# Performance work log

Hardware: AMD Instinct MI355X
Metric: run time of the kernel (lower is better)

## Reference

```python
import jax, jax.numpy as jnp
import numpy as np

IMG = 128                  # img_size
FMM = 35.0
SENSOR = 32.0
FUV = FMM * IMG / SENSOR   # focal length in pixels (screen space, in_ndc=False)
N_PTS = 16384
CHUNK = 1024               # points per scan step
R_SIL = 0.008              # silhouette pass radius (NDC)
R_DEP = 0.012              # depth pass radius (NDC)
K_SIL = 8
K_DEP = 16
DIST = 1.2


def _look_at(dist, elev_deg, azim_deg):
    # PyTorch3D look_at_view_transform with at=origin, up=+Y, degrees=True
    elev = jnp.deg2rad(elev_deg)
    azim = jnp.deg2rad(azim_deg)
    cam = jnp.stack([dist * jnp.cos(elev) * jnp.sin(azim),
                     dist * jnp.sin(elev),
                     dist * jnp.cos(elev) * jnp.cos(azim)], axis=-1)  # (B,3)
    up = jnp.array([0.0, 1.0, 0.0], dtype=cam.dtype)
    z_ax = -cam / (jnp.linalg.norm(cam, axis=-1, keepdims=True) + 1e-8)
    x_ax = jnp.cross(jnp.broadcast_to(up, z_ax.shape), z_ax)
    x_ax = x_ax / (jnp.linalg.norm(x_ax, axis=-1, keepdims=True) + 1e-8)
    y_ax = jnp.cross(z_ax, x_ax)
    R = jnp.stack([x_ax, y_ax, z_ax], axis=-1)   # columns are camera axes
    T = -jnp.einsum('bi,bij->bj', cam, R)        # X_cam = X_world @ R + T
    return R, T


def _project(pts, R, T):
    # world -> camera (row-vector convention) -> screen px -> PyTorch3D NDC
    Xc = jnp.einsum('bni,bij->bnj', pts, R) + T[:, None, :]
    z = Xc[..., 2]
    z_safe = jnp.where(z > 1e-5, z, 1.0)  # points behind camera are culled anyway
    xs = FUV * Xc[..., 0] / z_safe + IMG / 2.0
    ys = FUV * Xc[..., 1] / z_safe + IMG / 2.0
    x_ndc = 1.0 - 2.0 * xs / IMG
    y_ndc = 1.0 - 2.0 * ys / IMG
    return jnp.stack([x_ndc, y_ndc], axis=-1), z


def _rasterize(xy, z, r2, K):
    """Per-pixel K nearest-in-depth points within per-point NDC radius.
    xy: (B,N,2) NDC, z: (B,N) camera depth, r2: (B,N) squared radius.
    Returns zbuf, dists of shape (B,IMG,IMG,K), -1 for empty slots."""
    B, N, _ = xy.shape
    P = IMG * IMG
    # pixel-center NDC grid (PyTorch3D: +X left, +Y up; row-major flatten)
    gxs = 1.0 - (2.0 * jnp.arange(IMG, dtype=xy.dtype) + 1.0) / IMG  # per column
    gys = 1.0 - (2.0 * jnp.arange(IMG, dtype=xy.dtype) + 1.0) / IMG  # per row
    gx = jnp.tile(gxs, IMG)          # (P,)
    gy = jnp.repeat(gys, IMG)        # (P,)

    nch = N // CHUNK
    px = xy[..., 0].reshape(B, nch, CHUNK).swapaxes(0, 1)
    py = xy[..., 1].reshape(B, nch, CHUNK).swapaxes(0, 1)
    pz = z.reshape(B, nch, CHUNK).swapaxes(0, 1)
    pr2 = r2.reshape(B, nch, CHUNK).swapaxes(0, 1)

    def body(carry, c):
        top_z, top_d = carry
        cx, cy, cz, cr2 = c                               # each (B,CHUNK)
        dx = gx[None, :, None] - cx[:, None, :]           # (B,P,CHUNK)
        dy = gy[None, :, None] - cy[:, None, :]
        d2 = dx * dx + dy * dy
        ok = (d2 < cr2[:, None, :]) & (cz[:, None, :] > 0.0)
        zc = jnp.where(ok, cz[:, None, :], jnp.inf)
        cand_z = jnp.concatenate([top_z, zc], axis=-1)    # (B,P,K+CHUNK)
        cand_d = jnp.concatenate([top_d, d2], axis=-1)
        negz, idx = jax.lax.top_k(-cand_z, K)             # K smallest depths
        return (-negz, jnp.take_along_axis(cand_d, idx, axis=-1)), None

    init = (jnp.full((B, P, K), jnp.inf, dtype=xy.dtype),
            jnp.zeros((B, P, K), dtype=xy.dtype))
    (top_z, top_d), _ = jax.lax.scan(jax.checkpoint(body), init, (px, py, pz, pr2))
    valid = jnp.isfinite(top_z)
    zbuf = jnp.where(valid, top_z, -1.0).reshape(B, IMG, IMG, K)
    dists = jnp.where(valid, top_d, -1.0).reshape(B, IMG, IMG, K)
    return zbuf, dists


def setup_inputs() -> dict:
    key = jax.random.key(0)
    k1, k2 = jax.random.split(key)
    point_cloud = jax.random.normal(k1, (2, N_PTS, 6), dtype=jnp.float32) * 0.25
    param = jax.random.normal(k2, (2, 8, 3), dtype=jnp.float32) * 20.0  # degrees
    return {"point_cloud": point_cloud, "param": param}


def reference(point_cloud, param):
    pts = point_cloud[..., :3]
    B = pts.shape[0]
    elev0 = param[:, 1, 0]
    azim0 = param[:, 0, 0]

    # ---- silhouette pass (radius 0.008, K=8) + alpha compositing ----
    R0, T0 = _look_at(DIST, elev0, azim0)
    xy0, z0 = _project(pts, R0, T0)
    r2_sil = jnp.full((B, N_PTS), R_SIL * R_SIL, dtype=pts.dtype)
    _, dists_s = _rasterize(xy0, z0, r2_sil, K_SIL)
    alphas = jnp.where(dists_s >= 0.0, 1.0 - dists_s / (R_SIL * R_SIL), 0.0)
    trans = jnp.cumprod(1.0 - alphas, axis=-1)
    trans_excl = jnp.concatenate([jnp.ones_like(trans[..., :1]), trans[..., :-1]], axis=-1)
    sihlt_map = jnp.sum(alphas * trans_excl, axis=-1, keepdims=True) * 255.0  # (B,H,W,1)

    # ---- depth pass with random view (radius 0.012, K=16) ----
    kd = jax.random.key(42)
    ke, ka = jax.random.split(kd)
    elev_d = jax.random.uniform(ke, (B,), dtype=pts.dtype) * 60.0 - 30.0
    azim_d = jax.random.uniform(ka, (B,), dtype=pts.dtype) * 300.0 + azim0 + 30.0
    Rd, Td = _look_at(DIST, elev_d, azim_d)
    xyd, zd = _project(pts, Rd, Td)
    r2_dep = jnp.full((B, N_PTS), R_DEP * R_DEP, dtype=pts.dtype)
    zbuf_d, _ = _rasterize(xyd, zd, r2_dep, K_DEP)
    depth_ini = zbuf_d[..., 0]

    # density-aware adaptive radius (detached, per source .detach())
    area = jnp.sum((jax.lax.stop_gradient(depth_ini) > 0.0).astype(pts.dtype), axis=(1, 2))
    pa_radius = area / 16384.0 * 0.057                      # (B,)
    r2_ada = jnp.broadcast_to((pa_radius * pa_radius)[:, None], (B, N_PTS))

    zbuf_a, dists_a = _rasterize(xyd, zd, r2_ada, K_DEP)
    depth_img = zbuf_a[..., :8]
    dist_top = dists_a[..., :8]
    return (sihlt_map, depth_img, dist_top)
```

## Files before the change

kernel.cpp:

```cpp
#include <hip/hip_runtime.h>
#include <cstring>
#include <cstdint>

#define NPTS 16384
#define FUVC 140.0f
#define R_SILF 0.008f
#define R_DEPF 0.012f
#define R2_SIL (0.008f*0.008f)
#define R2_DEP (0.012f*0.012f)
#define CH 512

#define AREA_OFF  48
#define PA_OFF    50
#define R2ADA_OFF 52
#define CNT_SIL   64
#define OFF_SIL   2112
#define CNT_ADA   4160
#define OFF_ADA   6208
#define FLAGS8    8256
#define FLAGS     8256
#define ZERO_END  16448
#define PROJ0     41024
#define PROJ1     172096
#define LSILF     303168
#define LADAF     827456
#define WS1_WORDS 2007104u
#define WS1_NEEDED ((size_t)WS1_WORDS * 4u)
#define LSIL      303168
#define LADA      434240
#define WS2_WORDS 729152u
#define WS2_NEEDED ((size_t)WS2_WORDS * 4u)

__device__ __forceinline__ void cam_calc(float elev, float azim, float c[12]) {
    const float D2R = 0.017453292519943295f;
    float er = elev * D2R, ar = azim * D2R;
    float ce = cosf(er), se = sinf(er), ca = cosf(ar), sa = sinf(ar);
    float cx = 1.2f * ce * sa, cy = 1.2f * se, cz = 1.2f * ce * ca;
    float n = sqrtf(cx*cx + cy*cy + cz*cz) + 1e-8f;
    float zx = -cx / n, zy = -cy / n, zz = -cz / n;
    float xx = zz, xy = 0.0f, xz = -zx;
    float xn = sqrtf(xx*xx + xy*xy + xz*xz) + 1e-8f;
    xx /= xn; xz /= xn;
    float yx = zy*xz - zz*xy, yy = zz*xx - zx*xz, yz = zx*xy - zy*xx;
    c[0]=xx; c[1]=xy; c[2]=xz; c[3]=yx; c[4]=yy; c[5]=yz;
    c[6]=zx; c[7]=zy; c[8]=zz;
    c[9]  = -(cx*xx + cy*xy + cz*xz);
    c[10] = -(cx*yx + cy*yy + cz*yz);
    c[11] = -(cx*zx + cy*zy + cz*zz);
}

__device__ __forceinline__ void cam_compute(const float* __restrict__ param,
                                            float* __restrict__ ws,
                                            int t, float ue0, float ue1,
                                            float ua0, float ua1) {
    int b = t >> 1, cam = t & 1;
    float azim0 = param[b * 24 + 0];
    float elev0 = param[b * 24 + 3];
    float elev, azim;
    if (cam == 0) { elev = elev0; azim = azim0; }
    else {
        float ue = b ? ue1 : ue0;
        float ua = b ? ua1 : ua0;
        elev = ue * 60.0f - 30.0f;
        azim = ua * 300.0f + azim0 + 30.0f;
    }
    float c[12];
    cam_calc(elev, azim, c);
    float* w = ws + t * 12;
    #pragma unroll
    for (int i = 0; i < 12; i++) w[i] = c[i];
}

__device__ __forceinline__ float4 project_pt(const float* __restrict__ P,
                                             const float c[12]) {
    float X = P[0], Y = P[1], Z = P[2];
    float xc = X*c[0] + Y*c[1] + Z*c[2] + c[9];
    float yc = X*c[3] + Y*c[4] + Z*c[5] + c[10];
    float zc = X*c[6] + Y*c[7] + Z*c[8] + c[11];
    float zs = zc > 1e-5f ? zc : 1.0f;
    float px = 1.0f - (FUVC * xc / zs + 64.0f) * (1.0f/64.0f);
    float py = 1.0f - (FUVC * yc / zs + 64.0f) * (1.0f/64.0f);
    return make_float4(px, py, zc, 0.0f);
}

__device__ __forceinline__ void pix_range(float p, float r, int& lo, int& hi) {
    float lo_f = (1.0f - p - r) * 64.0f - 0.5f;
    float hi_f = (1.0f - p + r) * 64.0f - 0.5f;
    lo = (int)ceilf(lo_f - 1e-3f);
    hi = (int)floorf(hi_f + 1e-3f);
    lo = max(lo, 0); hi = min(hi, 127);
}

__device__ __forceinline__ void top8_insert(float z, float d,
                                            float tz[8], float td[8]) {
    #pragma unroll
    for (int k = 0; k < 8; k++) {
        bool lt = z < tz[k];
        float oz = tz[k], od = td[k];
        if (lt) { tz[k] = z; td[k] = d; z = oz; d = od; }
    }
}

__device__ __forceinline__ void hit_test(float4 pt, float gx, float gy, float r2,
                                         float tz[8], float td[8]) {
    float dx = gx - pt.x, dy = gy - pt.y;
    float d2 = dx*dx + dy*dy;
    if (d2 < r2 && pt.z > 0.0f && pt.z < tz[7]) top8_insert(pt.z, d2, tz, td);
}

__device__ __forceinline__ void merge_sorted8(float tz[8], float td[8], int mask) {
    float oz[8], od[8];
    #pragma unroll
    for (int k = 0; k < 8; k++) {
        oz[k] = __shfl_xor(tz[k], mask);
        od[k] = __shfl_xor(td[k], mask);
    }
    float mz[8], md[8];
    #pragma unroll
    for (int k = 0; k < 8; k++) {
        bool take = oz[7 - k] < tz[k];
        mz[k] = take ? oz[7 - k] : tz[k];
        md[k] = take ? od[7 - k] : td[k];
    }
    #define CE(i, j) { bool sw = mz[j] < mz[i]; \
        float t1 = mz[i], t2 = md[i]; \
        mz[i] = sw ? mz[j] : mz[i]; md[i] = sw ? md[j] : md[i]; \
        mz[j] = sw ? t1 : mz[j];    md[j] = sw ? t2 : md[j]; }
    CE(0,4) CE(1,5) CE(2,6) CE(3,7)
    CE(0,2) CE(1,3) CE(4,6) CE(5,7)
    CE(0,1) CE(2,3) CE(4,5) CE(6,7)
    #undef CE
    #pragma unroll
    for (int k = 0; k < 8; k++) { tz[k] = mz[k]; td[k] = md[k]; }
}

__device__ __forceinline__ void scan1024(unsigned* uw, unsigned cbase,
                                         unsigned obase, unsigned* s, int t) {
    unsigned c0 = uw[cbase + t*4 + 0];
    unsigned c1 = uw[cbase + t*4 + 1];
    unsigned c2 = uw[cbase + t*4 + 2];
    unsigned c3 = uw[cbase + t*4 + 3];
    unsigned tot = c0 + c1 + c2 + c3;
    s[t] = tot; __syncthreads();
    for (int off = 1; off < 256; off <<= 1) {
        unsigned v = (t >= off) ? s[t - off] : 0u;
        __syncthreads();
        s[t] += v;
        __syncthreads();
    }
    unsigned base = s[t] - tot;
    uw[obase + t*4 + 0] = base;
    uw[obase + t*4 + 1] = base + c0;
    uw[obase + t*4 + 2] = base + c0 + c1;
    uw[obase + t*4 + 3] = base + c0 + c1 + c2;
    uw[cbase + t*4 + 0] = 0;
    uw[cbase + t*4 + 1] = 0;
    uw[cbase + t*4 + 2] = 0;
    uw[cbase + t*4 + 3] = 0;
}


__global__ __launch_bounds__(256) void k_zero(float* __restrict__ ws) {
    unsigned* uw = (unsigned*)ws;
    int gid = blockIdx.x * 256 + threadIdx.x;
    int stride = gridDim.x * 256;
    for (int i = gid; i < ZERO_END; i += stride) uw[i] = 0u;
}

__global__ __launch_bounds__(256) void k_proj_v3(const float* __restrict__ pc,
                                                 const float* __restrict__ param,
                                                 float* __restrict__ ws,
                                                 float ue0, float ue1,
                                                 float ua0, float ua1) {
    unsigned* uw = (unsigned*)ws;
    unsigned char* fb = (unsigned char*)(uw + FLAGS8);
    int b = blockIdx.x >> 6;
    int p = ((blockIdx.x & 63) << 8) + threadIdx.x;
    const float* P = pc + ((size_t)b * NPTS + p) * 6;

    float azim0 = param[b * 24 + 0];
    float elev0 = param[b * 24 + 3];
    float c0[12], c1[12];
    cam_calc(elev0, azim0, c0);
    float ue = b ? ue1 : ue0;
    float ua = b ? ua1 : ua0;
    cam_calc(ue * 60.0f - 30.0f, ua * 300.0f + azim0 + 30.0f, c1);

    float4 q0 = project_pt(P, c0);
    ((float4*)(ws + PROJ0))[b * NPTS + p] = q0;
    if (q0.z > 0.0f) {
        int cl, chh, rl, rh;
        pix_range(q0.x, R_SILF, cl, chh);
        pix_range(q0.y, R_SILF, rl, rh);
        if (cl <= chh && rl <= rh) {
            int bxl = cl >> 2, bxh = chh >> 2, byl = rl >> 2, byh = rh >> 2;
            for (int by = byl; by <= byh; by++)
                for (int bx = bxl; bx <= bxh; bx++)
                    atomicAdd(&uw[CNT_SIL + b * 1024 + by * 32 + bx], 1u);
        }
    }

    float4 q1 = project_pt(P, c1);
    ((float4*)(ws + PROJ1))[b * NPTS + p] = q1;
    if (q1.z > 0.0f) {
        int cl, chh, rl, rh;
        pix_range(q1.x, R_DEPF, cl, chh);
        pix_range(q1.y, R_DEPF, rl, rh);
        for (int rr = rl; rr <= rh; rr++) {
            float gy = 1.0f - (float)(2 * rr + 1) * (1.0f/128.0f);
            float dy = gy - q1.y;
            for (int cc = cl; cc <= chh; cc++) {
                float gx = 1.0f - (float)(2 * cc + 1) * (1.0f/128.0f);
                float dx = gx - q1.x;
                float d2 = dx*dx + dy*dy;
                if (d2 < R2_DEP) fb[b * NPTS + rr * 128 + cc] = 1;
            }
        }
    }
}

__global__ __launch_bounds__(256) void k_area_scan_v3(float* __restrict__ ws) {
    unsigned* uw = (unsigned*)ws;
    __shared__ unsigned s[256];
    int t = threadIdx.x;
    int job = blockIdx.x;
    if (job < 2) {
        int b = job;
        unsigned acc = 0;
        #pragma unroll
        for (int j = 0; j < 16; j++) {
            unsigned w = uw[FLAGS8 + b * 4096 + t * 16 + j];
            acc += __popc(w & 0x01010101u);
        }
        s[t] = acc; __syncthreads();
        for (int off = 128; off > 0; off >>= 1) {
            if (t < off) s[t] += s[t + off];
            __syncthreads();
        }
        if (t == 0) {
            unsigned area = s[0];
            uw[AREA_OFF + b] = area;
            float pa = (float)area * (1.0f/16384.0f) * 0.057f;
            ws[PA_OFF + b] = pa;
            ws[R2ADA_OFF + b] = pa * pa;
        }
    } else {
        int b = job - 2;
        scan1024(uw, CNT_SIL + b * 1024, OFF_SIL + b * 1024, s, t);
    }
}

__global__ __launch_bounds__(64) void k_cntada_scatsil(float* __restrict__ ws) {
    unsigned* uw = (unsigned*)ws;
    int id = blockIdx.x;
    bool isCnt = id < 512;
    int p = ((isCnt ? id : id - 512) << 6) + threadIdx.x;
    int b = p >> 14;
    if (isCnt) {
        float4 q = ((const float4*)(ws + PROJ1))[p];
        float pa = ws[PA_OFF + b];
        if (q.z > 0.0f) {
            int cl, chh, rl, rh;
            pix_range(q.x, pa, cl, chh);
            pix_range(q.y, pa, rl, rh);
            if (cl <= chh && rl <= rh) {
                int bxl = cl >> 2, bxh = chh >> 2, byl = rl >> 2, byh = rh >> 2;
                for (int by = byl; by <= byh; by++)
                    for (int bx = bxl; bx <= bxh; bx++)
                        atomicAdd(&uw[CNT_ADA + b * 1024 + by * 32 + bx], 1u);
            }
        }
    } else {
        float4 q = ((const float4*)(ws + PROJ0))[p];
        if (q.z > 0.0f) {
            int cl, chh, rl, rh;
            pix_range(q.x, R_SILF, cl, chh);
            pix_range(q.y, R_SILF, rl, rh);
            if (cl <= chh && rl <= rh) {
                int bxl = cl >> 2, bxh = chh >> 2, byl = rl >> 2, byh = rh >> 2;
                for (int by = byl; by <= byh; by++)
                    for (int bx = bxl; bx <= bxh; bx++) {
                        unsigned bin = b * 1024 + by * 32 + bx;
                        unsigned idx = uw[OFF_SIL + bin] + atomicAdd(&uw[CNT_SIL + bin], 1u);
                        ((float4*)(ws + LSILF))[b * 65536 + idx] = q;
                    }
            }
        }
    }
}

__global__ __launch_bounds__(64) void k_scan_ada64(float* __restrict__ ws) {
    unsigned* uw = (unsigned*)ws;
    int b = blockIdx.x;
    int t = threadIdx.x;
    unsigned c[16]; unsigned tot = 0;
    #pragma unroll
    for (int j = 0; j < 16; j++) { c[j] = uw[CNT_ADA + b * 1024 + t * 16 + j]; tot += c[j]; }
    unsigned inc = tot;
    #pragma unroll
    for (int off = 1; off < 64; off <<= 1) {
        unsigned v = __shfl_up(inc, off);
        if (t >= off) inc += v;
    }
    unsigned base = inc - tot;
    #pragma unroll
    for (int j = 0; j < 16; j++) {
        uw[OFF_ADA + b * 1024 + t * 16 + j] = base;
        base += c[j];
        uw[CNT_ADA + b * 1024 + t * 16 + j] = 0u;
    }
}

__global__ __launch_bounds__(64) void k_scatter_ada_v2(float* __restrict__ ws) {
    unsigned* uw = (unsigned*)ws;
    int p = (blockIdx.x << 6) + threadIdx.x;
    int b = p >> 14;
    float4 q = ((const float4*)(ws + PROJ1))[p];
    float pa = ws[PA_OFF + b];
    if (q.z > 0.0f) {
        int cl, chh, rl, rh;
        pix_range(q.x, pa, cl, chh);
        pix_range(q.y, pa, rl, rh);
        if (cl <= chh && rl <= rh) {
            int bxl = cl >> 2, bxh = chh >> 2, byl = rl >> 2, byh = rh >> 2;
            for (int by = byl; by <= byh; by++)
                for (int bx = bxl; bx <= bxh; bx++) {
                    unsigned bin = b * 1024 + by * 32 + bx;
                    unsigned idx = uw[OFF_ADA + bin] + atomicAdd(&uw[CNT_ADA + bin], 1u);
                    ((float4*)(ws + LADAF))[b * 147456 + idx] = q;
                }
        }
    }
}

__global__ __launch_bounds__(64) void k_gather_v3(const float* __restrict__ ws,
                                                  float* __restrict__ out) {
    const unsigned* uw = (const unsigned*)ws;
    int id = blockIdx.x;
    bool sil = id < 2048;
    int gt = sil ? id : id - 2048;
    int b = gt >> 10;
    int tile = gt & 1023;
    int lane = threadIdx.x;
    int p = lane & 15, s = lane >> 4;
    int bx = tile & 31, by = tile >> 5;
    int col = (bx << 2) + (p & 3), row = (by << 2) + (p >> 2);
    float gx = 1.0f - (float)(2*col + 1) * (1.0f/128.0f);
    float gy = 1.0f - (float)(2*row + 1) * (1.0f/128.0f);
    float r2 = sil ? R2_SIL : ws[R2ADA_OFF + b];
    unsigned start = sil ? uw[OFF_SIL + b * 1024 + tile] : uw[OFF_ADA + b * 1024 + tile];
    unsigned len   = sil ? uw[CNT_SIL + b * 1024 + tile] : uw[CNT_ADA + b * 1024 + tile];
    const float4* lst = sil ? ((const float4*)(ws + LSILF)) + b * 65536 + start
                            : ((const float4*)(ws + LADAF)) + b * 147456 + start;

    float tz[8], td[8];
    #pragma unroll
    for (int k = 0; k < 8; k++) { tz[k] = INFINITY; td[k] = 0.0f; }

    unsigned i = (unsigned)s;
    while (i + 28 < len) {
        float4 cb[8];
        #pragma unroll
        for (int u = 0; u < 8; u++) cb[u] = lst[i + 4u * (unsigned)u];
        #pragma unroll
        for (int u = 0; u < 8; u++) hit_test(cb[u], gx, gy, r2, tz, td);
        i += 32;
    }
    for (; i < len; i += 4) hit_test(lst[i], gx, gy, r2, tz, td);

    merge_sorted8(tz, td, 16);
    merge_sorted8(tz, td, 32);

    if (s == 0) {
        int pix = (b << 14) + row * 128 + col;
        if (sil) {
            float trans = 1.0f, acc = 0.0f;
            #pragma unroll
            for (int k = 0; k < 8; k++) {
                float a = (tz[k] != INFINITY) ? (1.0f - td[k] / R2_SIL) : 0.0f;
                acc += a * trans;
                trans *= (1.0f - a);
            }
            out[pix] = acc * 255.0f;
        } else {
            float* dep = out + 32768  + (size_t)pix * 8;
            float* dst = out + 294912 + (size_t)pix * 8;
            #pragma unroll
            for (int k = 0; k < 8; k++) {
                bool v = (tz[k] != INFINITY);
                dep[k] = v ? tz[k] : -1.0f;
                dst[k] = v ? td[k] : -1.0f;
            }
        }
    }
}


__global__ __launch_bounds__(256) void k_init(const float* __restrict__ param,
                                              float* __restrict__ ws,
                                              float ue0, float ue1,
                                              float ua0, float ua1) {
    unsigned* uw = (unsigned*)ws;
    int gid = blockIdx.x * 256 + threadIdx.x;
    int stride = gridDim.x * 256;
    for (int i = gid; i < 2048; i += stride) { uw[CNT_SIL + i] = 0u; uw[CNT_ADA + i] = 0u; }
    for (int i = gid; i < 32768; i += stride) uw[FLAGS + i] = 0u;
    if (gid < 2) uw[AREA_OFF + gid] = 0u;
    if (gid < 4) cam_compute(param, ws, gid, ue0, ue1, ua0, ua1);
}

__global__ __launch_bounds__(256) void k_proj_count(const float* __restrict__ pc,
                                                    float* __restrict__ ws) {
    unsigned* uw = (unsigned*)ws;
    int b = blockIdx.x >> 6;
    int p = ((blockIdx.x & 63) << 8) + threadIdx.x;
    const float* P = pc + ((size_t)b * NPTS + p) * 6;
    float c0[12], c1[12];
    const float* w0 = ws + (b * 2) * 12;
    #pragma unroll
    for (int i = 0; i < 12; i++) { c0[i] = w0[i]; c1[i] = w0[12 + i]; }

    float4 q0 = project_pt(P, c0);
    ((float4*)(ws + PROJ0))[b * NPTS + p] = q0;
    if (q0.z > 0.0f) {
        int cl, chh, rl, rh;
        pix_range(q0.x, R_SILF, cl, chh);
        pix_range(q0.y, R_SILF, rl, rh);
        if (cl <= chh && rl <= rh) {
            int bxl = cl >> 2, bxh = chh >> 2, byl = rl >> 2, byh = rh >> 2;
            for (int by = byl; by <= byh; by++)
                for (int bx = bxl; bx <= bxh; bx++)
                    atomicAdd(&uw[CNT_SIL + b * 1024 + by * 32 + bx], 1u);
        }
    }

    float4 q1 = project_pt(P, c1);
    ((float4*)(ws + PROJ1))[b * NPTS + p] = q1;
    if (q1.z > 0.0f) {
        int cl, chh, rl, rh;
        pix_range(q1.x, R_DEPF, cl, chh);
        pix_range(q1.y, R_DEPF, rl, rh);
        for (int rr = rl; rr <= rh; rr++) {
            float gy = 1.0f - (float)(2 * rr + 1) * (1.0f/128.0f);
            float dy = gy - q1.y;
            for (int cc = cl; cc <= chh; cc++) {
                float gx = 1.0f - (float)(2 * cc + 1) * (1.0f/128.0f);
                float dx = gx - q1.x;
                float d2 = dx*dx + dy*dy;
                if (d2 < R2_DEP) uw[FLAGS + b * NPTS + rr * 128 + cc] = 1u;
            }
        }
    }
}

__global__ __launch_bounds__(256) void k_area_scan(float* __restrict__ ws) {
    unsigned* uw = (unsigned*)ws;
    __shared__ unsigned s[256];
    int t = threadIdx.x;
    int job = blockIdx.x;
    if (job < 2) {
        int b = job;
        unsigned acc = 0;
        for (int i = t; i < NPTS; i += 256) acc += uw[FLAGS + b * NPTS + i];
        s[t] = acc; __syncthreads();
        for (int off = 128; off > 0; off >>= 1) {
            if (t < off) s[t] += s[t + off];
            __syncthreads();
        }
        if (t == 0) {
            unsigned area = s[0];
            uw[AREA_OFF + b] = area;
            float pa = (float)area * (1.0f/16384.0f) * 0.057f;
            ws[PA_OFF + b] = pa;
            ws[R2ADA_OFF + b] = pa * pa;
        }
    } else {
        int b = job - 2;
        scan1024(uw, CNT_SIL + b * 1024, OFF_SIL + b * 1024, s, t);
    }
}

__global__ __launch_bounds__(256) void k_count_ada(float* __restrict__ ws) {
    unsigned* uw = (unsigned*)ws;
    int b = blockIdx.x >> 6;
    int p = ((blockIdx.x & 63) << 8) + threadIdx.x;
    float4 q = ((const float4*)(ws + PROJ1))[b * NPTS + p];
    float pa = ws[PA_OFF + b];
    if (q.z > 0.0f) {
        int cl, chh, rl, rh;
        pix_range(q.x, pa, cl, chh);
        pix_range(q.y, pa, rl, rh);
        if (cl <= chh && rl <= rh) {
            int bxl = cl >> 2, bxh = chh >> 2, byl = rl >> 2, byh = rh >> 2;
            for (int by = byl; by <= byh; by++)
                for (int bx = bxl; bx <= bxh; bx++)
                    atomicAdd(&uw[CNT_ADA + b * 1024 + by * 32 + bx], 1u);
        }
    }
}

__global__ __launch_bounds__(256) void k_scan_ada(float* __restrict__ ws) {
    unsigned* uw = (unsigned*)ws;
    __shared__ unsigned s[256];
    int b = blockIdx.x;
    scan1024(uw, CNT_ADA + b * 1024, OFF_ADA + b * 1024, s, threadIdx.x);
}

__global__ __launch_bounds__(256) void k_scatter(float* __restrict__ ws) {
    unsigned* uw = (unsigned*)ws;
    int b = blockIdx.x >> 6;
    int p = ((blockIdx.x & 63) << 8) + threadIdx.x;

    float4 q0 = ((const float4*)(ws + PROJ0))[b * NPTS + p];
    if (q0.z > 0.0f) {
        int cl, chh, rl, rh;
        pix_range(q0.x, R_SILF, cl, chh);
        pix_range(q0.y, R_SILF, rl, rh);
        if (cl <= chh && rl <= rh) {
            int bxl = cl >> 2, bxh = chh >> 2, byl = rl >> 2, byh = rh >> 2;
            for (int by = byl; by <= byh; by++)
                for (int bx = bxl; bx <= bxh; bx++) {
                    unsigned bin = b * 1024 + by * 32 + bx;
                    unsigned idx = uw[OFF_SIL + bin] + atomicAdd(&uw[CNT_SIL + bin], 1u);
                    uw[LSIL + b * 65536 + idx] = (unsigned)p;
                }
        }
    }

    float4 q1 = ((const float4*)(ws + PROJ1))[b * NPTS + p];
    float pa = ws[PA_OFF + b];
    if (q1.z > 0.0f) {
        int cl, chh, rl, rh;
        pix_range(q1.x, pa, cl, chh);
        pix_range(q1.y, pa, rl, rh);
        if (cl <= chh && rl <= rh) {
            int bxl = cl >> 2, bxh = chh >> 2, byl = rl >> 2, byh = rh >> 2;
            for (int by = byl; by <= byh; by++)
                for (int bx = bxl; bx <= bxh; bx++) {
                    unsigned bin = b * 1024 + by * 32 + bx;
                    unsigned idx = uw[OFF_ADA + bin] + atomicAdd(&uw[CNT_ADA + bin], 1u);
                    uw[LADA + b * 147456 + idx] = (unsigned)p;
                }
        }
    }
}

__global__ __launch_bounds__(256) void k_gather_sil(const float* __restrict__ ws,
                                                    float* __restrict__ out) {
    const unsigned* uw = (const unsigned*)ws;
    int b = blockIdx.x >> 6;
    int tile = (blockIdx.x & 63) * 16 + (threadIdx.x >> 4);
    int q = threadIdx.x & 15;
    int bx = tile & 31, by = tile >> 5;
    int col = (bx << 2) + (q & 3), row = (by << 2) + (q >> 2);
    float gx = 1.0f - (float)(2*col + 1) * (1.0f/128.0f);
    float gy = 1.0f - (float)(2*row + 1) * (1.0f/128.0f);
    unsigned start = uw[OFF_SIL + b * 1024 + tile];
    unsigned len   = uw[CNT_SIL + b * 1024 + tile];
    const float4* pr = (const float4*)(ws + PROJ0) + b * NPTS;

    float tz[8], td[8];
    #pragma unroll
    for (int k = 0; k < 8; k++) { tz[k] = INFINITY; td[k] = 0.0f; }
    for (unsigned i = 0; i < len; i++) {
        unsigned pid = uw[LSIL + b * 65536 + start + i];
        hit_test(pr[pid], gx, gy, R2_SIL, tz, td);
    }
    float trans = 1.0f, s = 0.0f;
    #pragma unroll
    for (int k = 0; k < 8; k++) {
        float a = (tz[k] != INFINITY) ? (1.0f - td[k] / R2_SIL) : 0.0f;
        s += a * trans;
        trans *= (1.0f - a);
    }
    out[(b << 14) + row * 128 + col] = s * 255.0f;
}

__global__ __launch_bounds__(256) void k_gather_ada(const float* __restrict__ ws,
                                                    float* __restrict__ out) {
    const unsigned* uw = (const unsigned*)ws;
    int b = blockIdx.x >> 6;
    int tile = (blockIdx.x & 63) * 16 + (threadIdx.x >> 4);
    int q = threadIdx.x & 15;
    int bx = tile & 31, by = tile >> 5;
    int col = (bx << 2) + (q & 3), row = (by << 2) + (q >> 2);
    float gx = 1.0f - (float)(2*col + 1) * (1.0f/128.0f);
    float gy = 1.0f - (float)(2*row + 1) * (1.0f/128.0f);
    float r2 = ws[R2ADA_OFF + b];
    unsigned start = uw[OFF_ADA + b * 1024 + tile];
    unsigned len   = uw[CNT_ADA + b * 1024 + tile];
    const float4* pr = (const float4*)(ws + PROJ1) + b * NPTS;

    float tz[8], td[8];
    #pragma unroll
    for (int k = 0; k < 8; k++) { tz[k] = INFINITY; td[k] = 0.0f; }
    for (unsigned i = 0; i < len; i++) {
        unsigned pid = uw[LADA + b * 147456 + start + i];
        hit_test(pr[pid], gx, gy, r2, tz, td);
    }
    int pix = (b << 14) + row * 128 + col;
    float* dep = out + 32768  + (size_t)pix * 8;
    float* dst = out + 294912 + (size_t)pix * 8;
    #pragma unroll
    for (int k = 0; k < 8; k++) {
        bool v = (tz[k] != INFINITY);
        dep[k] = v ? tz[k] : -1.0f;
        dst[k] = v ? td[k] : -1.0f;
    }
}

__global__ void cam_kernel_fb(const float* __restrict__ param, float* __restrict__ ws,
                              float ue0, float ue1, float ua0, float ua1) {
    int t = threadIdx.x;
    if (t < 2) ws[48 + t] = 0.0f;
    if (t >= 4) return;
    cam_compute(param, ws, t, ue0, ue1, ua0, ua1);
}

__device__ __forceinline__ void stage_points(const float* __restrict__ pcb,
                                             const float c[12], int c0, float4* sp) {
    for (int i = threadIdx.x; i < CH; i += 256) {
        const float* P = pcb + (size_t)(c0 + i) * 6;
        sp[i] = project_pt(P, c);
    }
}

__global__ __launch_bounds__(256) void raster_AB(const float* __restrict__ pc,
                                                 float* __restrict__ ws,
                                                 float* __restrict__ out) {
    __shared__ float4 sp[CH];
    int bid = blockIdx.x;
    bool silMode = bid < 128;
    int q = silMode ? bid : bid - 128;
    int b = q >> 6;
    int p = ((q & 63) << 8) + threadIdx.x;
    const float* cw = ws + (b * 2 + (silMode ? 0 : 1)) * 12;
    float c[12];
    #pragma unroll
    for (int i = 0; i < 12; i++) c[i] = cw[i];
    float r2 = silMode ? R2_SIL : R2_DEP;
    int col = p & 127, row = p >> 7;
    float gx = 1.0f - (float)(2*col + 1) * (1.0f/128.0f);
    float gy = 1.0f - (float)(2*row + 1) * (1.0f/128.0f);
    const float* pcb = pc + (size_t)b * NPTS * 6;

    if (silMode) {
        float tz[8], td[8];
        #pragma unroll
        for (int k = 0; k < 8; k++) { tz[k] = INFINITY; td[k] = 0.0f; }
        for (int c0 = 0; c0 < NPTS; c0 += CH) {
            __syncthreads();
            stage_points(pcb, c, c0, sp);
            __syncthreads();
            #pragma unroll 4
            for (int j = 0; j < CH; j++) hit_test(sp[j], gx, gy, r2, tz, td);
        }
        float trans = 1.0f, s = 0.0f;
        #pragma unroll
        for (int k = 0; k < 8; k++) {
            float a = (tz[k] != INFINITY) ? (1.0f - td[k] / r2) : 0.0f;
            s += a * trans;
            trans *= (1.0f - a);
        }
        out[(b << 14) + p] = s * 255.0f;
    } else {
        float mz = INFINITY;
        for (int c0 = 0; c0 < NPTS; c0 += CH) {
            __syncthreads();
            stage_points(pcb, c, c0, sp);
            __syncthreads();
            #pragma unroll 4
            for (int j = 0; j < CH; j++) {
                float4 pt = sp[j];
                float dx = gx - pt.x, dy = gy - pt.y;
                float d2 = dx*dx + dy*dy;
                if (d2 < r2 && pt.z > 0.0f) mz = fminf(mz, pt.z);
            }
        }
        unsigned long long m = __ballot(mz != INFINITY);
        if ((threadIdx.x & 63) == 0)
            atomicAdd(ws + 48 + b, (float)__popcll(m));
    }
}

__global__ __launch_bounds__(256) void raster_C(const float* __restrict__ pc,
                                                const float* __restrict__ ws,
                                                float* __restrict__ out) {
    __shared__ float4 sp[CH];
    int bid = blockIdx.x;
    int b = bid >> 6;
    int p = ((bid & 63) << 8) + threadIdx.x;
    const float* cw = ws + (b * 2 + 1) * 12;
    float c[12];
    #pragma unroll
    for (int i = 0; i < 12; i++) c[i] = cw[i];
    float area = ws[48 + b];
    float pa = (area * (1.0f/16384.0f)) * 0.057f;
    float r2 = pa * pa;
    int col = p & 127, row = p >> 7;
    float gx = 1.0f - (float)(2*col + 1) * (1.0f/128.0f);
    float gy = 1.0f - (float)(2*row + 1) * (1.0f/128.0f);
    const float* pcb = pc + (size_t)b * NPTS * 6;

    float tz[8], td[8];
    #pragma unroll
    for (int k = 0; k < 8; k++) { tz[k] = INFINITY; td[k] = 0.0f; }
    for (int c0 = 0; c0 < NPTS; c0 += CH) {
        __syncthreads();
        stage_points(pcb, c, c0, sp);
        __syncthreads();
        #pragma unroll 4
        for (int j = 0; j < CH; j++) hit_test(sp[j], gx, gy, r2, tz, td);
    }
    float* dep = out + 32768  + (size_t)((b << 14) + p) * 8;
    float* dst = out + 294912 + (size_t)((b << 14) + p) * 8;
    #pragma unroll
    for (int k = 0; k < 8; k++) {
        bool v = (tz[k] != INFINITY);
        dep[k] = v ? tz[k] : -1.0f;
        dst[k] = v ? td[k] : -1.0f;
    }
}

static inline uint32_t rotl32(uint32_t x, int r) { return (x << r) | (x >> (32 - r)); }

static void tf2x32(uint32_t k0, uint32_t k1, uint32_t c0, uint32_t c1,
                   uint32_t* o0, uint32_t* o1) {
    uint32_t ks0 = k0, ks1 = k1, ks2 = k0 ^ k1 ^ 0x1BD11BDAu;
    uint32_t x0 = c0 + ks0, x1 = c1 + ks1;
    static const int rA[4] = {13, 15, 26, 6};
    static const int rB[4] = {17, 29, 16, 24};
    #define RND4(R) do { for (int i = 0; i < 4; i++) { x0 += x1; x1 = rotl32(x1, R[i]); x1 ^= x0; } } while (0)
    RND4(rA); x0 += ks1; x1 += ks2 + 1u;
    RND4(rB); x0 += ks2; x1 += ks0 + 2u;
    RND4(rA); x0 += ks0; x1 += ks1 + 3u;
    RND4(rB); x0 += ks1; x1 += ks2 + 4u;
    RND4(rA); x0 += ks2; x1 += ks0 + 5u;
    #undef RND4
    *o0 = x0; *o1 = x1;
}

static inline float bits_to_unit_float(uint32_t bits) {
    uint32_t fb = (bits >> 9) | 0x3f800000u;
    float f;
    memcpy(&f, &fb, 4);
    return f - 1.0f;
}

extern "C" void kernel_launch(void* const* d_in, const int* in_sizes, int n_in,
                              void* d_out, int out_size, void* d_ws, size_t ws_size,
                              hipStream_t stream) {
    const float* pc    = (const float*)d_in[0];
    const float* param = (const float*)d_in[1];
    float* out = (float*)d_out;
    float* ws  = (float*)d_ws;

    uint32_t ke0, ke1, ka0, ka1, b1, b2;
    tf2x32(0u, 42u, 0u, 0u, &ke0, &ke1);
    tf2x32(0u, 42u, 0u, 1u, &ka0, &ka1);
    float ue[2], ua[2];
    for (uint32_t i = 0; i < 2; i++) {
        tf2x32(ke0, ke1, 0u, i, &b1, &b2);
        ue[i] = bits_to_unit_float(b1 ^ b2);
        tf2x32(ka0, ka1, 0u, i, &b1, &b2);
        ua[i] = bits_to_unit_float(b1 ^ b2);
    }

    if (ws_size >= WS1_NEEDED) {
        k_zero          <<<16, 256, 0, stream>>>(ws);
        k_proj_v3       <<<128, 256, 0, stream>>>(pc, param, ws, ue[0], ue[1], ua[0], ua[1]);
        k_area_scan_v3  <<<4, 256, 0, stream>>>(ws);
        k_cntada_scatsil<<<1024, 64, 0, stream>>>(ws);
        k_scan_ada64    <<<2, 64, 0, stream>>>(ws);
        k_scatter_ada_v2<<<512, 64, 0, stream>>>(ws);
        k_gather_v3     <<<4096, 64, 0, stream>>>(ws, out);
    } else if (ws_size >= WS2_NEEDED) {
        k_init      <<<64, 256, 0, stream>>>(param, ws, ue[0], ue[1], ua[0], ua[1]);
        k_proj_count<<<128, 256, 0, stream>>>(pc, ws);
        k_area_scan <<<4, 256, 0, stream>>>(ws);
        k_count_ada <<<128, 256, 0, stream>>>(ws);
        k_scan_ada  <<<2, 256, 0, stream>>>(ws);
        k_scatter   <<<128, 256, 0, stream>>>(ws);
        k_gather_sil<<<128, 256, 0, stream>>>(ws, out);
        k_gather_ada<<<128, 256, 0, stream>>>(ws, out);
    } else {
        cam_kernel_fb<<<1, 64, 0, stream>>>(param, ws, ue[0], ue[1], ua[0], ua[1]);
        raster_AB<<<256, 256, 0, stream>>>(pc, ws, out);
        raster_C <<<128, 256, 0, stream>>>(pc, ws, out);
    }
}
```

Before: 96.44 us.

## Fuse seven-kernel pipeline into one cooperative kernel with grid syncs

Replaces the chain of seven kernel launches (zero, project, area/scan, count/scatter, scan, scatter, gather) with a single cooperative kernel of 1024 blocks that separates the stages with grid.sync(). The goal is to remove per-launch overhead and inter-kernel gaps, which dominate a workload this small. In exchange it adds grid-wide barrier cost, runs many idle threads in the serial scan stages, and queries device properties and occupancy on the host every call. It falls back to the old launches if cooperative launch is unavailable.

```diff
diff --git a/kernel.cpp b/kernel.cpp
--- a/kernel.cpp
+++ b/kernel.cpp
@@ -1,6 +1,9 @@
 #include <hip/hip_runtime.h>
+#include <hip/hip_cooperative_groups.h>
 #include <cstring>
 #include <cstdint>
+
+namespace cg = cooperative_groups;
 
 #define NPTS 16384
 #define FUVC 140.0f
@@ -31,6 +34,9 @@
 #define WS2_WORDS 729152u
 #define WS2_NEEDED ((size_t)WS2_WORDS * 4u)
 
+#define FUSED_BLOCKS 1024
+#define FUSED_NT (FUSED_BLOCKS * 256)
+
 __device__ __forceinline__ void cam_calc(float elev, float azim, float c[12]) {
     const float D2R = 0.017453292519943295f;
     float er = elev * D2R, ar = azim * D2R;
@@ -159,32 +165,15 @@
     uw[cbase + t*4 + 3] = 0;
 }
 
-
-__global__ __launch_bounds__(256) void k_zero(float* __restrict__ ws) {
-    unsigned* uw = (unsigned*)ws;
-    int gid = blockIdx.x * 256 + threadIdx.x;
-    int stride = gridDim.x * 256;
-    for (int i = gid; i < ZERO_END; i += stride) uw[i] = 0u;
-}
-
-__global__ __launch_bounds__(256) void k_proj_v3(const float* __restrict__ pc,
-                                                 const float* __restrict__ param,
-                                                 float* __restrict__ ws,
-                                                 float ue0, float ue1,
-                                                 float ua0, float ua1) {
+__device__ __forceinline__ void body_proj(const float* __restrict__ pc,
+                                          float* __restrict__ ws, int b, int p) {
     unsigned* uw = (unsigned*)ws;
     unsigned char* fb = (unsigned char*)(uw + FLAGS8);
-    int b = blockIdx.x >> 6;
-    int p = ((blockIdx.x & 63) << 8) + threadIdx.x;
     const float* P = pc + ((size_t)b * NPTS + p) * 6;
-
-    float azim0 = param[b * 24 + 0];
-    float elev0 = param[b * 24 + 3];
     float c0[12], c1[12];
-    cam_calc(elev0, azim0, c0);
-    float ue = b ? ue1 : ue0;
-    float ua = b ? ua1 : ua0;
-    cam_calc(ue * 60.0f - 30.0f, ua * 300.0f + azim0 + 30.0f, c1);
+    const float* w0 = ws + (b * 2) * 12;
+    #pragma unroll
+    for (int i = 0; i < 12; i++) { c0[i] = w0[i]; c1[i] = w0[12 + i]; }
 
     float4 q0 = project_pt(P, c0);
     ((float4*)(ws + PROJ0))[b * NPTS + p] = q0;
@@ -219,11 +208,9 @@
     }
 }
 
-__global__ __launch_bounds__(256) void k_area_scan_v3(float* __restrict__ ws) {
-    unsigned* uw = (unsigned*)ws;
-    __shared__ unsigned s[256];
-    int t = threadIdx.x;
-    int job = blockIdx.x;
+__device__ __forceinline__ void body_area_scan(float* __restrict__ ws, int job,
+                                               int t, unsigned* s) {
+    unsigned* uw = (unsigned*)ws;
     if (job < 2) {
         int b = job;
         unsigned acc = 0;
@@ -250,49 +237,46 @@
     }
 }
 
-__global__ __launch_bounds__(64) void k_cntada_scatsil(float* __restrict__ ws) {
-    unsigned* uw = (unsigned*)ws;
-    int id = blockIdx.x;
-    bool isCnt = id < 512;
-    int p = ((isCnt ? id : id - 512) << 6) + threadIdx.x;
+__device__ __forceinline__ void body_cnt_ada(float* __restrict__ ws, int p) {
+    unsigned* uw = (unsigned*)ws;
     int b = p >> 14;
-    if (isCnt) {
-        float4 q = ((const float4*)(ws + PROJ1))[p];
-        float pa = ws[PA_OFF + b];
-        if (q.z > 0.0f) {
-            int cl, chh, rl, rh;
-            pix_range(q.x, pa, cl, chh);
-            pix_range(q.y, pa, rl, rh);
-            if (cl <= chh && rl <= rh) {
-                int bxl = cl >> 2, bxh = chh >> 2, byl = rl >> 2, byh = rh >> 2;
-                for (int by = byl; by <= byh; by++)
-                    for (int bx = bxl; bx <= bxh; bx++)
-                        atomicAdd(&uw[CNT_ADA + b * 1024 + by * 32 + bx], 1u);
-            }
-        }
-    } else {
-        float4 q = ((const float4*)(ws + PROJ0))[p];
-        if (q.z > 0.0f) {
-            int cl, chh, rl, rh;
-            pix_range(q.x, R_SILF, cl, chh);
-            pix_range(q.y, R_SILF, rl, rh);
-            if (cl <= chh && rl <= rh) {
-                int bxl = cl >> 2, bxh = chh >> 2, byl = rl >> 2, byh = rh >> 2;
-                for (int by = byl; by <= byh; by++)
-                    for (int bx = bxl; bx <= bxh; bx++) {
-                        unsigned bin = b * 1024 + by * 32 + bx;
-                        unsigned idx = uw[OFF_SIL + bin] + atomicAdd(&uw[CNT_SIL + bin], 1u);
-                        ((float4*)(ws + LSILF))[b * 65536 + idx] = q;
-                    }
-            }
-        }
-    }
-}
-
-__global__ __launch_bounds__(64) void k_scan_ada64(float* __restrict__ ws) {
-    unsigned* uw = (unsigned*)ws;
-    int b = blockIdx.x;
-    int t = threadIdx.x;
+    float4 q = ((const float4*)(ws + PROJ1))[p];
+    float pa = ws[PA_OFF + b];
+    if (q.z > 0.0f) {
+        int cl, chh, rl, rh;
+        pix_range(q.x, pa, cl, chh);
+        pix_range(q.y, pa, rl, rh);
+        if (cl <= chh && rl <= rh) {
+            int bxl = cl >> 2, bxh = chh >> 2, byl = rl >> 2, byh = rh >> 2;
+            for (int by = byl; by <= byh; by++)
+                for (int bx = bxl; bx <= bxh; bx++)
+                    atomicAdd(&uw[CNT_ADA + b * 1024 + by * 32 + bx], 1u);
+        }
+    }
+}
+
+__device__ __forceinline__ void body_scat_sil(float* __restrict__ ws, int p) {
+    unsigned* uw = (unsigned*)ws;
+    int b = p >> 14;
+    float4 q = ((const float4*)(ws + PROJ0))[p];
+    if (q.z > 0.0f) {
+        int cl, chh, rl, rh;
+        pix_range(q.x, R_SILF, cl, chh);
+        pix_range(q.y, R_SILF, rl, rh);
+        if (cl <= chh && rl <= rh) {
+            int bxl = cl >> 2, bxh = chh >> 2, byl = rl >> 2, byh = rh >> 2;
+            for (int by = byl; by <= byh; by++)
+                for (int bx = bxl; bx <= bxh; bx++) {
+                    unsigned bin = b * 1024 + by * 32 + bx;
+                    unsigned idx = uw[OFF_SIL + bin] + atomicAdd(&uw[CNT_SIL + bin], 1u);
+                    ((float4*)(ws + LSILF))[b * 65536 + idx] = q;
+                }
+        }
+    }
+}
+
+__device__ __forceinline__ void body_scan_ada(float* __restrict__ ws, int b, int t) {
+    unsigned* uw = (unsigned*)ws;
     unsigned c[16]; unsigned tot = 0;
     #pragma unroll
     for (int j = 0; j < 16; j++) { c[j] = uw[CNT_ADA + b * 1024 + t * 16 + j]; tot += c[j]; }
@@ -311,9 +295,8 @@
     }
 }
 
-__global__ __launch_bounds__(64) void k_scatter_ada_v2(float* __restrict__ ws) {
-    unsigned* uw = (unsigned*)ws;
-    int p = (blockIdx.x << 6) + threadIdx.x;
+__device__ __forceinline__ void body_scat_ada(float* __restrict__ ws, int p) {
+    unsigned* uw = (unsigned*)ws;
     int b = p >> 14;
     float4 q = ((const float4*)(ws + PROJ1))[p];
     float pa = ws[PA_OFF + b];
@@ -333,15 +316,14 @@
     }
 }
 
-__global__ __launch_bounds__(64) void k_gather_v3(const float* __restrict__ ws,
-                                                  float* __restrict__ out) {
+__device__ __forceinline__ void body_gather(const float* __restrict__ ws,
+                                            float* __restrict__ out,
+                                            int id, int lane) {
     const unsigned* uw = (const unsigned*)ws;
-    int id = blockIdx.x;
     bool sil = id < 2048;
     int gt = sil ? id : id - 2048;
     int b = gt >> 10;
     int tile = gt & 1023;
-    int lane = threadIdx.x;
     int p = lane & 15, s = lane >> 4;
     int bx = tile & 31, by = tile >> 5;
     int col = (bx << 2) + (p & 3), row = (by << 2) + (p >> 2);
@@ -395,30 +377,67 @@
     }
 }
 
-
-__global__ __launch_bounds__(256) void k_init(const float* __restrict__ param,
-                                              float* __restrict__ ws,
-                                              float ue0, float ue1,
-                                              float ua0, float ua1) {
+__global__ __launch_bounds__(256) void k_fused(const float* __restrict__ pc,
+                                               const float* __restrict__ param,
+                                               float* __restrict__ ws,
+                                               float* __restrict__ out,
+                                               float ue0, float ue1,
+                                               float ua0, float ua1) {
+    cg::grid_group grid = cg::this_grid();
+    unsigned* uw = (unsigned*)ws;
+    __shared__ unsigned s[256];
+    int tid = blockIdx.x * 256 + threadIdx.x;
+
+    for (int i = 48 + tid; i < ZERO_END; i += FUSED_NT) uw[i] = 0u;
+    if (tid < 4) cam_compute(param, ws, tid, ue0, ue1, ua0, ua1);
+    grid.sync();
+
+    if (tid < 2 * NPTS) body_proj(pc, ws, tid >> 14, tid & (NPTS - 1));
+    grid.sync();
+
+    if (blockIdx.x < 4) body_area_scan(ws, blockIdx.x, threadIdx.x, s);
+    grid.sync();
+
+    if (tid < 2 * NPTS) body_cnt_ada(ws, tid);
+    else if (tid < 4 * NPTS) body_scat_sil(ws, tid - 2 * NPTS);
+    grid.sync();
+
+    if (blockIdx.x == 0 && threadIdx.x < 128)
+        body_scan_ada(ws, threadIdx.x >> 6, threadIdx.x & 63);
+    grid.sync();
+
+    if (tid < 2 * NPTS) body_scat_ada(ws, tid);
+    grid.sync();
+
+    body_gather(ws, out, tid >> 6, tid & 63);
+}
+
+
+__global__ __launch_bounds__(256) void k_zero(float* __restrict__ ws) {
     unsigned* uw = (unsigned*)ws;
     int gid = blockIdx.x * 256 + threadIdx.x;
     int stride = gridDim.x * 256;
-    for (int i = gid; i < 2048; i += stride) { uw[CNT_SIL + i] = 0u; uw[CNT_ADA + i] = 0u; }
-    for (int i = gid; i < 32768; i += stride) uw[FLAGS + i] = 0u;
-    if (gid < 2) uw[AREA_OFF + gid] = 0u;
-    if (gid < 4) cam_compute(param, ws, gid, ue0, ue1, ua0, ua1);
-}
-
-__global__ __launch_bounds__(256) void k_proj_count(const float* __restrict__ pc,
-                                                    float* __restrict__ ws) {
-    unsigned* uw = (unsigned*)ws;
+    for (int i = gid; i < ZERO_END; i += stride) uw[i] = 0u;
+}
+
+__global__ __launch_bounds__(256) void k_proj_v3(const float* __restrict__ pc,
+                                                 const float* __restrict__ param,
+                                                 float* __restrict__ ws,
+                                                 float ue0, float ue1,
+                                                 float ua0, float ua1) {
     int b = blockIdx.x >> 6;
     int p = ((blockIdx.x & 63) << 8) + threadIdx.x;
+    float azim0 = param[b * 24 + 0];
+    float elev0 = param[b * 24 + 3];
+    float c0[12], c1[12];
+    cam_calc(elev0, azim0, c0);
+    float ue = b ? ue1 : ue0;
+    float ua = b ? ua1 : ua0;
+    cam_calc(ue * 60.0f - 30.0f, ua * 300.0f + azim0 + 30.0f, c1);
+
+    unsigned* uw = (unsigned*)ws;
+    unsigned char* fb = (unsigned char*)(uw + FLAGS8);
     const float* P = pc + ((size_t)b * NPTS + p) * 6;
-    float c0[12], c1[12];
-    const float* w0 = ws + (b * 2) * 12;
-    #pragma unroll
-    for (int i = 0; i < 12; i++) { c0[i] = w0[i]; c1[i] = w0[12 + i]; }
 
     float4 q0 = project_pt(P, c0);
     ((float4*)(ws + PROJ0))[b * NPTS + p] = q0;
@@ -433,7 +452,89 @@
                     atomicAdd(&uw[CNT_SIL + b * 1024 + by * 32 + bx], 1u);
         }
     }
-
+    float4 q1 = project_pt(P, c1);
+    ((float4*)(ws + PROJ1))[b * NPTS + p] = q1;
+    if (q1.z > 0.0f) {
+        int cl, chh, rl, rh;
+        pix_range(q1.x, R_DEPF, cl, chh);
+        pix_range(q1.y, R_DEPF, rl, rh);
+        for (int rr = rl; rr <= rh; rr++) {
+            float gy = 1.0f - (float)(2 * rr + 1) * (1.0f/128.0f);
+            float dy = gy - q1.y;
+            for (int cc = cl; cc <= chh; cc++) {
+                float gx = 1.0f - (float)(2 * cc + 1) * (1.0f/128.0f);
+                float dx = gx - q1.x;
+                float d2 = dx*dx + dy*dy;
+                if (d2 < R2_DEP) fb[b * NPTS + rr * 128 + cc] = 1;
+            }
+        }
+    }
+}
+
+__global__ __launch_bounds__(256) void k_area_scan_v3(float* __restrict__ ws) {
+    __shared__ unsigned s[256];
+    body_area_scan(ws, blockIdx.x, threadIdx.x, s);
+}
+
+__global__ __launch_bounds__(64) void k_cntada_scatsil(float* __restrict__ ws) {
+    int id = blockIdx.x;
+    bool isCnt = id < 512;
+    int p = ((isCnt ? id : id - 512) << 6) + threadIdx.x;
+    if (isCnt) body_cnt_ada(ws, p);
+    else       body_scat_sil(ws, p);
+}
+
+__global__ __launch_bounds__(64) void k_scan_ada64(float* __restrict__ ws) {
+    body_scan_ada(ws, blockIdx.x, threadIdx.x);
+}
+
+__global__ __launch_bounds__(64) void k_scatter_ada_v2(float* __restrict__ ws) {
+    body_scat_ada(ws, (blockIdx.x << 6) + threadIdx.x);
+}
+
+__global__ __launch_bounds__(64) void k_gather_v3(const float* __restrict__ ws,
+                                                  float* __restrict__ out) {
+    body_gather(ws, out, blockIdx.x, threadIdx.x);
+}
+
+
+__global__ __launch_bounds__(256) void k_init(const float* __restrict__ param,
+                                              float* __restrict__ ws,
+                                              float ue0, float ue1,
+                                              float ua0, float ua1) {
+    unsigned* uw = (unsigned*)ws;
+    int gid = blockIdx.x * 256 + threadIdx.x;
+    int stride = gridDim.x * 256;
+    for (int i = gid; i < 2048; i += stride) { uw[CNT_SIL + i] = 0u; uw[CNT_ADA + i] = 0u; }
+    for (int i = gid; i < 32768; i += stride) uw[FLAGS + i] = 0u;
+    if (gid < 2) uw[AREA_OFF + gid] = 0u;
+    if (gid < 4) cam_compute(param, ws, gid, ue0, ue1, ua0, ua1);
+}
+
+__global__ __launch_bounds__(256) void k_proj_count(const float* __restrict__ pc,
+                                                    float* __restrict__ ws) {
+    unsigned* uw = (unsigned*)ws;
+    int b = blockIdx.x >> 6;
+    int p = ((blockIdx.x & 63) << 8) + threadIdx.x;
+    const float* P = pc + ((size_t)b * NPTS + p) * 6;
+    float c0[12], c1[12];
+    const float* w0 = ws + (b * 2) * 12;
+    #pragma unroll
+    for (int i = 0; i < 12; i++) { c0[i] = w0[i]; c1[i] = w0[12 + i]; }
+
+    float4 q0 = project_pt(P, c0);
+    ((float4*)(ws + PROJ0))[b * NPTS + p] = q0;
+    if (q0.z > 0.0f) {
+        int cl, chh, rl, rh;
+        pix_range(q0.x, R_SILF, cl, chh);
+        pix_range(q0.y, R_SILF, rl, rh);
+        if (cl <= chh && rl <= rh) {
+            int bxl = cl >> 2, bxh = chh >> 2, byl = rl >> 2, byh = rh >> 2;
+            for (int by = byl; by <= byh; by++)
+                for (int bx = bxl; bx <= bxh; bx++)
+                    atomicAdd(&uw[CNT_SIL + b * 1024 + by * 32 + bx], 1u);
+        }
+    }
     float4 q1 = project_pt(P, c1);
     ((float4*)(ws + PROJ1))[b * NPTS + p] = q1;
     if (q1.z > 0.0f) {
@@ -526,7 +627,6 @@
                 }
         }
     }
-
     float4 q1 = ((const float4*)(ws + PROJ1))[b * NPTS + p];
     float pa = ws[PA_OFF + b];
     if (q1.z > 0.0f) {
@@ -765,17 +865,38 @@
         tf2x32(ka0, ka1, 0u, i, &b1, &b2);
         ua[i] = bits_to_unit_float(b1 ^ b2);
     }
+    float ue0 = ue[0], ue1 = ue[1], ua0 = ua[0], ua1 = ua[1];
 
     if (ws_size >= WS1_NEEDED) {
+        int dev = 0;
+        hipGetDevice(&dev);
+        hipDeviceProp_t prop;
+        bool coop = (hipGetDeviceProperties(&prop, dev) == hipSuccess) &&
+                    prop.cooperativeLaunch;
+        if (coop) {
+            int maxB = 0;
+            if (hipOccupancyMaxActiveBlocksPerMultiprocessor(&maxB, k_fused, 256, 0)
+                    != hipSuccess ||
+                maxB * prop.multiProcessorCount < FUSED_BLOCKS)
+                coop = false;
+        }
+        if (coop) {
+            void* args[] = { (void*)&pc, (void*)&param, (void*)&ws, (void*)&out,
+                             (void*)&ue0, (void*)&ue1, (void*)&ua0, (void*)&ua1 };
+            hipError_t e = hipLaunchCooperativeKernel((const void*)k_fused,
+                                                      dim3(FUSED_BLOCKS), dim3(256),
+                                                      args, 0, stream);
+            if (e == hipSuccess) return;
+        }
         k_zero          <<<16, 256, 0, stream>>>(ws);
-        k_proj_v3       <<<128, 256, 0, stream>>>(pc, param, ws, ue[0], ue[1], ua[0], ua[1]);
+        k_proj_v3       <<<128, 256, 0, stream>>>(pc, param, ws, ue0, ue1, ua0, ua1);
         k_area_scan_v3  <<<4, 256, 0, stream>>>(ws);
         k_cntada_scatsil<<<1024, 64, 0, stream>>>(ws);
         k_scan_ada64    <<<2, 64, 0, stream>>>(ws);
         k_scatter_ada_v2<<<512, 64, 0, stream>>>(ws);
         k_gather_v3     <<<4096, 64, 0, stream>>>(ws, out);
     } else if (ws_size >= WS2_NEEDED) {
-        k_init      <<<64, 256, 0, stream>>>(param, ws, ue[0], ue[1], ua[0], ua[1]);
+        k_init      <<<64, 256, 0, stream>>>(param, ws, ue0, ue1, ua0, ua1);
         k_proj_count<<<128, 256, 0, stream>>>(pc, ws);
         k_area_scan <<<4, 256, 0, stream>>>(ws);
         k_count_ada <<<128, 256, 0, stream>>>(ws);
@@ -784,7 +905,7 @@
         k_gather_sil<<<128, 256, 0, stream>>>(ws, out);
         k_gather_ada<<<128, 256, 0, stream>>>(ws, out);
     } else {
-        cam_kernel_fb<<<1, 64, 0, stream>>>(param, ws, ue[0], ue[1], ua[0], ua[1]);
+        cam_kernel_fb<<<1, 64, 0, stream>>>(param, ws, ue0, ue1, ua0, ua1);
         raster_AB<<<256, 256, 0, stream>>>(pc, ws, out);
         raster_C <<<128, 256, 0, stream>>>(pc, ws, out);
     }
```

Result: faster. 92.22 us (-4.4%).
